# Optimization experiments

Measured on AMD Instinct MI355X. Metric: run time of the kernel, lower is better.

Reference implementation:

```python
import jax, jax.numpy as jnp
import numpy as np

B, S, H, I, E, K = 1, 2048, 1024, 2048, 8, 2


def setup_inputs() -> dict:
    key = jax.random.key(0)
    k0, k1, k2, k3, k4 = jax.random.split(key, 5)
    x = jax.random.normal(k0, (B, S, H), dtype=jnp.float32)
    Wg = jax.random.normal(k1, (H, E), dtype=jnp.float32) * 0.02   # gate (no bias)
    W1 = jax.random.normal(k2, (E, H, I), dtype=jnp.float32) * 0.02  # expert up
    W3 = jax.random.normal(k3, (E, H, I), dtype=jnp.float32) * 0.02  # expert gate
    W2 = jax.random.normal(k4, (E, I, H), dtype=jnp.float32) * 0.02  # expert down
    return {"x": x, "Wg": Wg, "W1": W1, "W2": W2, "W3": W3}


def reference(x, Wg, W1, W2, W3):
    b, s, h = x.shape
    e = Wg.shape[1]
    xf = x.reshape(-1, h)                      # (T, H)
    T = xf.shape[0]

    # Router: top-2 logits, softmax over the 2 selected logits (fp32), cast back.
    logits = xf @ Wg                           # (T, E)
    top_vals, top_idx = jax.lax.top_k(logits, K)
    rw = jax.nn.softmax(top_vals.astype(jnp.float32), axis=-1).astype(x.dtype)  # (T, K)

    # Dense per-expert combine weight: w[t, e] = routing weight if expert e selected, else 0.
    w = jnp.zeros((T, e), dtype=x.dtype).at[jnp.arange(T)[:, None], top_idx].add(rw)

    # Expert MLPs computed for all experts, zero-weighted tokens contribute nothing
    # (mathematically identical to the gather/MLP/scatter-add in the torch loop).
    up = jnp.einsum('th,ehi->tei', xf, W1)     # (T, E, I)
    gate = jnp.einsum('th,ehi->tei', xf, W3)   # (T, E, I)
    act = jax.nn.silu(up) * gate               # (T, E, I)
    out = jnp.einsum('tei,eih,te->th', act, W2, w)  # (T, H)
    return out.reshape(b, s, h)
```

## Files before the change

### kernel.cpp

```cpp
#include <hip/hip_runtime.h>
#include <math.h>

#define NUM_TOK 2048
#define HDIM 1024
#define IDIM 2048
#define NEXP 8
#define MAX_ROWS 5120
#define NTM 40

typedef __attribute__((ext_vector_type(8))) short bf16x8;
typedef __attribute__((ext_vector_type(4))) float f32x4;

#define OFF_IDX   0u
#define OFF_RW    16384u
#define OFF_SEG   32832u
#define OFF_ROWS  33024u
#define OFF_POS   53504u
#define OFF_XB    131072u
#define OFF_ACT   109051904u
#define OFF_SO    8388608u

__device__ __forceinline__ unsigned short f2bf(float f) {
  union { float f; unsigned u; } v; v.f = f;
  unsigned r = v.u + 0x7FFF + ((v.u >> 16) & 1);
  return (unsigned short)(r >> 16);
}

__device__ __forceinline__ unsigned pk2(float lo, float hi) {
  return (unsigned)f2bf(lo) | ((unsigned)f2bf(hi) << 16);
}

__device__ __forceinline__ void gld16(const void* g, void* l) {
  __builtin_amdgcn_global_load_lds(
      (const __attribute__((address_space(1))) void*)g,
      (__attribute__((address_space(3))) void*)l, 16, 0, 0);
}


__global__ void k_router(const float* __restrict__ x, const float* __restrict__ wg,
                         unsigned short* __restrict__ xb,
                         int* __restrict__ idx, float* __restrict__ rw) {
  const int wave = threadIdx.x >> 6, lane = threadIdx.x & 63;
  const int t = blockIdx.x * 4 + wave;
  const float2* __restrict__ xr = (const float2*)(x + (size_t)t * HDIM);
  unsigned* __restrict__ xbr = (unsigned*)(xb + (size_t)t * HDIM);
  float acc[8];
#pragma unroll
  for (int q = 0; q < 8; ++q) acc[q] = 0.f;
#pragma unroll
  for (int j = 0; j < 8; ++j) {
    const int h2 = lane + (j << 6);
    const float2 v = xr[h2];
    const float* wrow = wg + (size_t)h2 * 16;
    const float4 a0 = *(const float4*)(wrow);
    const float4 a1 = *(const float4*)(wrow + 4);
    const float4 b0 = *(const float4*)(wrow + 8);
    const float4 b1 = *(const float4*)(wrow + 12);
    acc[0] = fmaf(v.x, a0.x, fmaf(v.y, b0.x, acc[0]));
    acc[1] = fmaf(v.x, a0.y, fmaf(v.y, b0.y, acc[1]));
    acc[2] = fmaf(v.x, a0.z, fmaf(v.y, b0.z, acc[2]));
    acc[3] = fmaf(v.x, a0.w, fmaf(v.y, b0.w, acc[3]));
    acc[4] = fmaf(v.x, a1.x, fmaf(v.y, b1.x, acc[4]));
    acc[5] = fmaf(v.x, a1.y, fmaf(v.y, b1.y, acc[5]));
    acc[6] = fmaf(v.x, a1.z, fmaf(v.y, b1.z, acc[6]));
    acc[7] = fmaf(v.x, a1.w, fmaf(v.y, b1.w, acc[7]));
    xbr[h2] = pk2(v.x, v.y);
  }
#pragma unroll
  for (int q = 0; q < 8; ++q) {
#pragma unroll
    for (int off = 32; off >= 1; off >>= 1)
      acc[q] += __shfl_xor(acc[q], off, 64);
  }
  if (lane == 0) {
    int i0 = 0; float v0 = acc[0];
#pragma unroll
    for (int q = 1; q < 8; ++q)
      if (acc[q] > v0) { v0 = acc[q]; i0 = q; }
    int i1 = -1; float v1 = -3.4e38f;
#pragma unroll
    for (int q = 0; q < 8; ++q)
      if (q != i0 && acc[q] > v1) { v1 = acc[q]; i1 = q; }
    const float e1 = expf(v1 - v0);
    const float inv = 1.f / (1.f + e1);
    idx[2 * t] = i0; idx[2 * t + 1] = i1;
    rw[2 * t] = inv; rw[2 * t + 1] = e1 * inv;
  }
}

__global__ void k_segscatter(const int* __restrict__ idx, int* __restrict__ seg,
                             int* __restrict__ rowsv, int* __restrict__ pos) {
  __shared__ int hist[NEXP], cur[NEXP], sseg[NEXP];
  const int tid = threadIdx.x;
  if (tid < NEXP) { hist[tid] = 0; cur[tid] = 0; }
  __syncthreads();
  for (int s = tid; s < 2 * NUM_TOK; s += 256) atomicAdd(&hist[idx[s]], 1);
  for (int r = tid; r < MAX_ROWS; r += 256) rowsv[r] = -1;
  __syncthreads();
  if (tid == 0) {
    int s = 0;
    for (int q = 0; q < NEXP; ++q) {
      seg[q] = s; sseg[q] = s;
      s += ((hist[q] + 127) / 128) * 128;
    }
    seg[NEXP] = s;
  }
  __syncthreads();
  for (int s = tid; s < 2 * NUM_TOK; s += 256) {
    const int e = idx[s];
    const int p = atomicAdd(&cur[e], 1);
    const int rr = sseg[e] + p;
    rowsv[rr] = s;
    pos[s] = rr;
  }
}

__launch_bounds__(256, 2)
__global__ void k_gemm1(const unsigned short* __restrict__ xb,
                        const float* __restrict__ W1f,
                        const float* __restrict__ W3f,
                        const int* __restrict__ seg, const int* __restrict__ rowsv,
                        unsigned short* __restrict__ act) {
  __shared__ __align__(16) unsigned short As[2][128 * 32];
  __shared__ __align__(16) unsigned short Bs[2][128 * 32];
  const int tid = threadIdx.x;
  const int w = tid >> 6, l = tid & 63;
  const int m0 = blockIdx.y * 128;
  const int total = seg[NEXP];
  if (m0 >= total) return;
  int e = 0;
#pragma unroll
  for (int q = 1; q < NEXP; ++q) if (m0 >= seg[q]) e = q;
  const int n0 = blockIdx.x * 64;

  const int swzA = ((l & 3) ^ ((l >> 4) & 3) ^ ((l >> 3) & 3)) * 8;
  size_t aOff[2];
#pragma unroll
  for (int q = 0; q < 2; ++q) {
    const int r = rowsv[m0 + w * 32 + q * 16 + (l >> 2)];
    const int tk = (r < 0) ? 0 : (r >> 1);
    aOff[q] = (size_t)tk * HDIM + swzA;
  }
  const int kk = tid >> 4;
  const int ng = tid & 15;
  const size_t bBase = (size_t)e * HDIM * IDIM + (size_t)(2 * kk) * IDIM + n0 + ng * 4;
  float4 u0, u1, g0, g1;
  auto loadB = [&](int k0) {
    const size_t b = bBase + (size_t)k0 * IDIM;
    u0 = *(const float4*)(W1f + b);
    u1 = *(const float4*)(W1f + b + IDIM);
    g0 = *(const float4*)(W3f + b);
    g1 = *(const float4*)(W3f + b + IDIM);
  };
  auto writeB = [&](int buf) {
    unsigned* Bd = (unsigned*)&Bs[buf][0];
    const float a0[4] = {u0.x, u0.y, u0.z, u0.w};
    const float a1[4] = {u1.x, u1.y, u1.z, u1.w};
    const float c0[4] = {g0.x, g0.y, g0.z, g0.w};
    const float c1[4] = {g1.x, g1.y, g1.z, g1.w};
#pragma unroll
    for (int i = 0; i < 4; ++i) {
      const int r = ng * 4 + i;
      const int f = ((r >> 2) & 3) ^ ((r >> 1) & 3);
      const int d = (((kk >> 2) ^ f) << 2) + (kk & 3);
      Bd[r * 16 + d]        = pk2(a0[i], a1[i]);
      Bd[(r + 64) * 16 + d] = pk2(c0[i], c1[i]);
    }
  };
  auto stageA = [&](int buf, int k0) {
#pragma unroll
    for (int q = 0; q < 2; ++q)
      gld16(xb + aOff[q] + k0, &As[buf][(w * 32 + q * 16) * 32]);
  };

  f32x4 acc[2][8];
#pragma unroll
  for (int m = 0; m < 2; ++m)
#pragma unroll
    for (int nf = 0; nf < 8; ++nf) acc[m][nf] = (f32x4)0.f;

  stageA(0, 0);
  loadB(0);
  writeB(0);
  __syncthreads();

  const int rslot = ((l >> 4) ^ ((l >> 2) & 3) ^ ((l >> 1) & 3)) * 8;
  const int arow = (w * 32 + (l & 15)) * 32 + rslot;
  const int NT = HDIM / 32;
  for (int t = 0; t < NT; ++t) {
    const int cur = t & 1;
    if (t + 1 < NT) { stageA(cur ^ 1, (t + 1) * 32); loadB((t + 1) * 32); }
    __builtin_amdgcn_sched_barrier(0);
    const bf16x8 a0 = *(const bf16x8*)&As[cur][arow];
    const bf16x8 a1 = *(const bf16x8*)&As[cur][arow + 16 * 32];
#pragma unroll
    for (int nf = 0; nf < 8; ++nf) {
      const bf16x8 b = *(const bf16x8*)&Bs[cur][(nf * 16 + (l & 15)) * 32 + rslot];
      acc[0][nf] = __builtin_amdgcn_mfma_f32_16x16x32_bf16(a0, b, acc[0][nf], 0, 0, 0);
      acc[1][nf] = __builtin_amdgcn_mfma_f32_16x16x32_bf16(a1, b, acc[1][nf], 0, 0, 0);
    }
    if (t + 1 < NT) writeB(cur ^ 1);
    __syncthreads();
  }
  const int rbase = m0 + w * 32 + (l >> 4) * 4;
  const int cbase = n0 + (l & 15);
#pragma unroll
  for (int m = 0; m < 2; ++m)
#pragma unroll
    for (int p = 0; p < 4; ++p) {
      const f32x4 up = acc[m][p];
      const f32x4 gt = acc[m][p + 4];
#pragma unroll
      for (int r = 0; r < 4; ++r) {
        const float u = up[r];
        const float s = (u / (1.f + expf(-u))) * gt[r];
        act[(size_t)(rbase + m * 16 + r) * IDIM + cbase + p * 16] = f2bf(s);
      }
    }
}

__launch_bounds__(256, 2)
__global__ void k_gemm2(const unsigned short* __restrict__ act,
                        const float* __restrict__ W2f,
                        const int* __restrict__ seg,
                        float* __restrict__ so) {
  __shared__ __align__(16) unsigned short As[2][128 * 32];
  __shared__ __align__(16) unsigned short Bs[2][128 * 32];
  const int tid = threadIdx.x;
  const int w = tid >> 6, l = tid & 63;
  const int m0 = blockIdx.y * 128;
  const int total = seg[NEXP];
  if (m0 >= total) return;
  int e = 0;
#pragma unroll
  for (int q = 1; q < NEXP; ++q) if (m0 >= seg[q]) e = q;
  const int n0 = blockIdx.x * 128;

  const int swzA = ((tid & 3) ^ ((tid >> 4) & 3) ^ ((tid >> 3) & 3)) * 8;
  size_t aOff[2];
#pragma unroll
  for (int q = 0; q < 2; ++q)
    aOff[q] = (size_t)(m0 + q * 64 + (tid >> 2)) * IDIM + swzA;

  const int kk = tid >> 4;
  const int ng = tid & 15;
  const size_t bBase = (size_t)e * IDIM * HDIM + (size_t)(2 * kk) * HDIM + n0 + ng * 4;
  float4 v0[2], v1[2];
  auto loadB = [&](int k0) {
#pragma unroll
    for (int q = 0; q < 2; ++q) {
      const size_t b = bBase + (size_t)k0 * HDIM + q * 64;
      v0[q] = *(const float4*)(W2f + b);
      v1[q] = *(const float4*)(W2f + b + HDIM);
    }
  };
  auto writeB = [&](int buf) {
    unsigned* Bd = (unsigned*)&Bs[buf][0];
#pragma unroll
    for (int q = 0; q < 2; ++q) {
      const float a0[4] = {v0[q].x, v0[q].y, v0[q].z, v0[q].w};
      const float a1[4] = {v1[q].x, v1[q].y, v1[q].z, v1[q].w};
#pragma unroll
      for (int i = 0; i < 4; ++i) {
        const int rm = ng * 4 + i;
        const int f = ((rm >> 2) & 3) ^ ((rm >> 1) & 3);
        const int d = (((kk >> 2) ^ f) << 2) + (kk & 3);
        Bd[(q * 64 + rm) * 16 + d] = pk2(a0[i], a1[i]);
      }
    }
  };
  auto stageA = [&](int buf, int k0) {
#pragma unroll
    for (int q = 0; q < 2; ++q)
      gld16(act + aOff[q] + k0, &As[buf][(q * 64 + (tid >> 2)) * 32]);
  };

  f32x4 acc[2][8];
#pragma unroll
  for (int mf = 0; mf < 2; ++mf)
#pragma unroll
    for (int nf = 0; nf < 8; ++nf) acc[mf][nf] = (f32x4)0.f;

  stageA(0, 0);
  loadB(0);
  writeB(0);
  __syncthreads();

  const int rslot = ((l >> 4) ^ ((l >> 2) & 3) ^ ((l >> 1) & 3)) * 8;
  const int arow = (w * 32 + (l & 15)) * 32 + rslot;
  const int NT = IDIM / 32;
  for (int t = 0; t < NT; ++t) {
    const int cur = t & 1;
    if (t + 1 < NT) { stageA(cur ^ 1, (t + 1) * 32); loadB((t + 1) * 32); }
    __builtin_amdgcn_sched_barrier(0);
    const bf16x8 a0 = *(const bf16x8*)&As[cur][arow];
    const bf16x8 a1 = *(const bf16x8*)&As[cur][arow + 16 * 32];
#pragma unroll
    for (int nf = 0; nf < 8; ++nf) {
      const bf16x8 b = *(const bf16x8*)&Bs[cur][(nf * 16 + (l & 15)) * 32 + rslot];
      acc[0][nf] = __builtin_amdgcn_mfma_f32_16x16x32_bf16(a0, b, acc[0][nf], 0, 0, 0);
      acc[1][nf] = __builtin_amdgcn_mfma_f32_16x16x32_bf16(a1, b, acc[1][nf], 0, 0, 0);
    }
    if (t + 1 < NT) writeB(cur ^ 1);
    __syncthreads();
  }
  const int rbase = m0 + w * 32 + (l >> 4) * 4;
  const int cbase = n0 + (l & 15);
#pragma unroll
  for (int mf = 0; mf < 2; ++mf)
#pragma unroll
    for (int nf = 0; nf < 8; ++nf)
#pragma unroll
      for (int r = 0; r < 4; ++r)
        so[(size_t)(rbase + mf * 16 + r) * HDIM + cbase + nf * 16] = acc[mf][nf][r];
}

__global__ void k_combine(const float* __restrict__ so, const int* __restrict__ pos,
                          const float* __restrict__ rw, float* __restrict__ out) {
  const int t = blockIdx.x, i = threadIdx.x;
  const int p0 = pos[2 * t], p1 = pos[2 * t + 1];
  const float w0 = rw[2 * t], w1 = rw[2 * t + 1];
  const float4 a = ((const float4*)(so + (size_t)p0 * HDIM))[i];
  const float4 b = ((const float4*)(so + (size_t)p1 * HDIM))[i];
  float4 o;
  o.x = w0 * a.x + w1 * b.x;
  o.y = w0 * a.y + w1 * b.y;
  o.z = w0 * a.z + w1 * b.z;
  o.w = w0 * a.w + w1 * b.w;
  ((float4*)(out + (size_t)t * HDIM))[i] = o;
}

extern "C" void kernel_launch(void* const* d_in, const int* in_sizes, int n_in,
                              void* d_out, int out_size, void* d_ws, size_t ws_size,
                              hipStream_t stream) {
  const float* x  = (const float*)d_in[0];
  const float* Wg = (const float*)d_in[1];
  const float* W1 = (const float*)d_in[2];
  const float* W2 = (const float*)d_in[3];
  const float* W3 = (const float*)d_in[4];
  float* out = (float*)d_out;
  char* ws = (char*)d_ws;
  int*   idx  = (int*)(ws + OFF_IDX);
  float* rw   = (float*)(ws + OFF_RW);
  int*   seg  = (int*)(ws + OFF_SEG);
  int*   rowsv= (int*)(ws + OFF_ROWS);
  int*   pos  = (int*)(ws + OFF_POS);
  unsigned short* xb  = (unsigned short*)(ws + OFF_XB);
  unsigned short* act = (unsigned short*)(ws + OFF_ACT);
  float* so = (float*)(ws + OFF_SO);

  k_router<<<NUM_TOK / 4, 256, 0, stream>>>(x, Wg, xb, idx, rw);
  k_segscatter<<<1, 256, 0, stream>>>(idx, seg, rowsv, pos);
  k_gemm1<<<dim3(IDIM / 64, NTM), 256, 0, stream>>>(xb, W1, W3, seg, rowsv, act);
  k_gemm2<<<dim3(HDIM / 128, NTM), 256, 0, stream>>>(act, W2, seg, so);
  k_combine<<<NUM_TOK, 256, 0, stream>>>(so, pos, rw, out);
}
```

Measured before the change: 166.5 us.

## Deepen weight prefetch to two tiles ahead and use native bf16 conversion

Both expert GEMM kernels now keep two register sets of fp32 weights in flight and unroll the K loop by two, so global weight loads are issued two tiles ahead of their LDS write. This is meant to hide more global-load latency behind the MFMA work. The manual round-to-nearest bf16 packing is replaced with the compiler's native __bf16 cast, which may map to a hardware convert instruction. In exchange the kernels use more registers, which could lower occupancy.

```diff
diff --git a/kernel.cpp b/kernel.cpp
--- a/kernel.cpp
+++ b/kernel.cpp
@@ -21,13 +21,14 @@
 #define OFF_SO    8388608u
 
 __device__ __forceinline__ unsigned short f2bf(float f) {
-  union { float f; unsigned u; } v; v.f = f;
-  unsigned r = v.u + 0x7FFF + ((v.u >> 16) & 1);
-  return (unsigned short)(r >> 16);
+  __bf16 b = (__bf16)f;
+  return __builtin_bit_cast(unsigned short, b);
 }
 
 __device__ __forceinline__ unsigned pk2(float lo, float hi) {
-  return (unsigned)f2bf(lo) | ((unsigned)f2bf(hi) << 16);
+  __bf16 a = (__bf16)lo, b = (__bf16)hi;
+  return (unsigned)__builtin_bit_cast(unsigned short, a) |
+         ((unsigned)__builtin_bit_cast(unsigned short, b) << 16);
 }
 
 __device__ __forceinline__ void gld16(const void* g, void* l) {
@@ -144,20 +145,21 @@
   const int kk = tid >> 4;
   const int ng = tid & 15;
   const size_t bBase = (size_t)e * HDIM * IDIM + (size_t)(2 * kk) * IDIM + n0 + ng * 4;
-  float4 u0, u1, g0, g1;
-  auto loadB = [&](int k0) {
+
+  struct Bregs { float4 u0, u1, g0, g1; };
+  auto loadB = [&](Bregs& p, int k0) {
     const size_t b = bBase + (size_t)k0 * IDIM;
-    u0 = *(const float4*)(W1f + b);
-    u1 = *(const float4*)(W1f + b + IDIM);
-    g0 = *(const float4*)(W3f + b);
-    g1 = *(const float4*)(W3f + b + IDIM);
-  };
-  auto writeB = [&](int buf) {
+    p.u0 = *(const float4*)(W1f + b);
+    p.u1 = *(const float4*)(W1f + b + IDIM);
+    p.g0 = *(const float4*)(W3f + b);
+    p.g1 = *(const float4*)(W3f + b + IDIM);
+  };
+  auto writeB = [&](int buf, const Bregs& p) {
     unsigned* Bd = (unsigned*)&Bs[buf][0];
-    const float a0[4] = {u0.x, u0.y, u0.z, u0.w};
-    const float a1[4] = {u1.x, u1.y, u1.z, u1.w};
-    const float c0[4] = {g0.x, g0.y, g0.z, g0.w};
-    const float c1[4] = {g1.x, g1.y, g1.z, g1.w};
+    const float a0[4] = {p.u0.x, p.u0.y, p.u0.z, p.u0.w};
+    const float a1[4] = {p.u1.x, p.u1.y, p.u1.z, p.u1.w};
+    const float c0[4] = {p.g0.x, p.g0.y, p.g0.z, p.g0.w};
+    const float c1[4] = {p.g1.x, p.g1.y, p.g1.z, p.g1.w};
 #pragma unroll
     for (int i = 0; i < 4; ++i) {
       const int r = ng * 4 + i;
@@ -179,27 +181,39 @@
 #pragma unroll
     for (int nf = 0; nf < 8; ++nf) acc[m][nf] = (f32x4)0.f;
 
-  stageA(0, 0);
-  loadB(0);
-  writeB(0);
-  __syncthreads();
-
   const int rslot = ((l >> 4) ^ ((l >> 2) & 3) ^ ((l >> 1) & 3)) * 8;
   const int arow = (w * 32 + (l & 15)) * 32 + rslot;
-  const int NT = HDIM / 32;
-  for (int t = 0; t < NT; ++t) {
-    const int cur = t & 1;
-    if (t + 1 < NT) { stageA(cur ^ 1, (t + 1) * 32); loadB((t + 1) * 32); }
-    __builtin_amdgcn_sched_barrier(0);
-    const bf16x8 a0 = *(const bf16x8*)&As[cur][arow];
-    const bf16x8 a1 = *(const bf16x8*)&As[cur][arow + 16 * 32];
+  auto mfmaStep = [&](int buf) {
+    const bf16x8 a0 = *(const bf16x8*)&As[buf][arow];
+    const bf16x8 a1 = *(const bf16x8*)&As[buf][arow + 16 * 32];
 #pragma unroll
     for (int nf = 0; nf < 8; ++nf) {
-      const bf16x8 b = *(const bf16x8*)&Bs[cur][(nf * 16 + (l & 15)) * 32 + rslot];
+      const bf16x8 b = *(const bf16x8*)&Bs[buf][(nf * 16 + (l & 15)) * 32 + rslot];
       acc[0][nf] = __builtin_amdgcn_mfma_f32_16x16x32_bf16(a0, b, acc[0][nf], 0, 0, 0);
       acc[1][nf] = __builtin_amdgcn_mfma_f32_16x16x32_bf16(a1, b, acc[1][nf], 0, 0, 0);
     }
-    if (t + 1 < NT) writeB(cur ^ 1);
+  };
+
+  Bregs pA, pB;
+  loadB(pA, 0);
+  stageA(0, 0);
+  loadB(pB, 32);
+  writeB(0, pA);
+  __syncthreads();
+
+  const int NT = HDIM / 32;
+  for (int t = 0; t < NT; t += 2) {
+    if (t + 2 < NT) loadB(pA, (t + 2) * 32);
+    stageA(1, (t + 1) * 32);
+    __builtin_amdgcn_sched_barrier(0);
+    mfmaStep(0);
+    writeB(1, pB);
+    __syncthreads();
+    if (t + 3 < NT) loadB(pB, (t + 3) * 32);
+    if (t + 2 < NT) stageA(0, (t + 2) * 32);
+    __builtin_amdgcn_sched_barrier(0);
+    mfmaStep(1);
+    if (t + 2 < NT) writeB(0, pA);
     __syncthreads();
   }
   const int rbase = m0 + w * 32 + (l >> 4) * 4;
@@ -245,28 +259,28 @@
   const int kk = tid >> 4;
   const int ng = tid & 15;
   const size_t bBase = (size_t)e * IDIM * HDIM + (size_t)(2 * kk) * HDIM + n0 + ng * 4;
-  float4 v0[2], v1[2];
-  auto loadB = [&](int k0) {
-#pragma unroll
-    for (int q = 0; q < 2; ++q) {
-      const size_t b = bBase + (size_t)k0 * HDIM + q * 64;
-      v0[q] = *(const float4*)(W2f + b);
-      v1[q] = *(const float4*)(W2f + b + HDIM);
-    }
-  };
-  auto writeB = [&](int buf) {
+
+  struct Bregs { float4 a0, a1, b0, b1; };
+  auto loadB = [&](Bregs& p, int k0) {
+    const size_t b = bBase + (size_t)k0 * HDIM;
+    p.a0 = *(const float4*)(W2f + b);
+    p.a1 = *(const float4*)(W2f + b + HDIM);
+    p.b0 = *(const float4*)(W2f + b + 64);
+    p.b1 = *(const float4*)(W2f + b + HDIM + 64);
+  };
+  auto writeB = [&](int buf, const Bregs& p) {
     unsigned* Bd = (unsigned*)&Bs[buf][0];
-#pragma unroll
-    for (int q = 0; q < 2; ++q) {
-      const float a0[4] = {v0[q].x, v0[q].y, v0[q].z, v0[q].w};
-      const float a1[4] = {v1[q].x, v1[q].y, v1[q].z, v1[q].w};
-#pragma unroll
-      for (int i = 0; i < 4; ++i) {
-        const int rm = ng * 4 + i;
-        const int f = ((rm >> 2) & 3) ^ ((rm >> 1) & 3);
-        const int d = (((kk >> 2) ^ f) << 2) + (kk & 3);
-        Bd[(q * 64 + rm) * 16 + d] = pk2(a0[i], a1[i]);
-      }
+    const float q00[4] = {p.a0.x, p.a0.y, p.a0.z, p.a0.w};
+    const float q01[4] = {p.a1.x, p.a1.y, p.a1.z, p.a1.w};
+    const float q10[4] = {p.b0.x, p.b0.y, p.b0.z, p.b0.w};
+    const float q11[4] = {p.b1.x, p.b1.y, p.b1.z, p.b1.w};
+#pragma unroll
+    for (int i = 0; i < 4; ++i) {
+      const int rm = ng * 4 + i;
+      const int f = ((rm >> 2) & 3) ^ ((rm >> 1) & 3);
+      const int d = (((kk >> 2) ^ f) << 2) + (kk & 3);
+      Bd[rm * 16 + d]        = pk2(q00[i], q01[i]);
+      Bd[(rm + 64) * 16 + d] = pk2(q10[i], q11[i]);
     }
   };
   auto stageA = [&](int buf, int k0) {
@@ -281,27 +295,39 @@
 #pragma unroll
     for (int nf = 0; nf < 8; ++nf) acc[mf][nf] = (f32x4)0.f;
 
-  stageA(0, 0);
-  loadB(0);
-  writeB(0);
-  __syncthreads();
-
   const int rslot = ((l >> 4) ^ ((l >> 2) & 3) ^ ((l >> 1) & 3)) * 8;
   const int arow = (w * 32 + (l & 15)) * 32 + rslot;
-  const int NT = IDIM / 32;
-  for (int t = 0; t < NT; ++t) {
-    const int cur = t & 1;
-    if (t + 1 < NT) { stageA(cur ^ 1, (t + 1) * 32); loadB((t + 1) * 32); }
-    __builtin_amdgcn_sched_barrier(0);
-    const bf16x8 a0 = *(const bf16x8*)&As[cur][arow];
-    const bf16x8 a1 = *(const bf16x8*)&As[cur][arow + 16 * 32];
+  auto mfmaStep = [&](int buf) {
+    const bf16x8 a0 = *(const bf16x8*)&As[buf][arow];
+    const bf16x8 a1 = *(const bf16x8*)&As[buf][arow + 16 * 32];
 #pragma unroll
     for (int nf = 0; nf < 8; ++nf) {
-      const bf16x8 b = *(const bf16x8*)&Bs[cur][(nf * 16 + (l & 15)) * 32 + rslot];
+      const bf16x8 b = *(const bf16x8*)&Bs[buf][(nf * 16 + (l & 15)) * 32 + rslot];
       acc[0][nf] = __builtin_amdgcn_mfma_f32_16x16x32_bf16(a0, b, acc[0][nf], 0, 0, 0);
       acc[1][nf] = __builtin_amdgcn_mfma_f32_16x16x32_bf16(a1, b, acc[1][nf], 0, 0, 0);
     }
-    if (t + 1 < NT) writeB(cur ^ 1);
+  };
+
+  Bregs pA, pB;
+  loadB(pA, 0);
+  stageA(0, 0);
+  loadB(pB, 32);
+  writeB(0, pA);
+  __syncthreads();
+
+  const int NT = IDIM / 32;
+  for (int t = 0; t < NT; t += 2) {
+    if (t + 2 < NT) loadB(pA, (t + 2) * 32);
+    stageA(1, (t + 1) * 32);
+    __builtin_amdgcn_sched_barrier(0);
+    mfmaStep(0);
+    writeB(1, pB);
+    __syncthreads();
+    if (t + 3 < NT) loadB(pB, (t + 3) * 32);
+    if (t + 2 < NT) stageA(0, (t + 2) * 32);
+    __builtin_amdgcn_sched_barrier(0);
+    mfmaStep(1);
+    if (t + 2 < NT) writeB(0, pA);
     __syncthreads();
   }
   const int rbase = m0 + w * 32 + (l >> 4) * 4;
```

Result: faster. 161.3 us (-3.1%).
